# Optimization experiments

Hardware: AMD Instinct MI355X
Metric: run time of the kernel (lower is better)

Reference implementation:

```python
import jax, jax.numpy as jnp
import numpy as np

B, C, H, W = 4, 64, 64, 64

def setup_inputs() -> dict:
    key = jax.random.key(0)
    ks = jax.random.split(key, 8)
    s = 1.0 / np.sqrt(C)
    return {
        "x": jax.random.normal(ks[0], (B, C, H, W), dtype=jnp.float32),
        "Wq": jax.random.normal(ks[1], (C, C), dtype=jnp.float32) * s,
        "bq": jax.random.normal(ks[2], (C,), dtype=jnp.float32) * s,
        "Wk": jax.random.normal(ks[3], (C, C), dtype=jnp.float32) * s,
        "bk": jax.random.normal(ks[4], (C,), dtype=jnp.float32) * s,
        "Wv": jax.random.normal(ks[5], (C, C), dtype=jnp.float32) * s,
        "bv": jax.random.normal(ks[6], (C,), dtype=jnp.float32) * s,
        "gamma": jax.random.normal(ks[7], (1,), dtype=jnp.float32),
    }

def reference(x, Wq, bq, Wk, bk, Wv, bv, gamma):
    b, c, h, w = x.shape
    xf = x.reshape(b, c, h * w)                      # [B, C, N]
    q = jnp.einsum('oc,bcn->bon', Wq, xf) + bq[None, :, None]
    k = jnp.einsum('oc,bcn->bon', Wk, xf) + bk[None, :, None]
    v = jnp.einsum('oc,bcn->bon', Wv, xf) + bv[None, :, None]
    energy = jnp.einsum('bci,bcj->bij', q, k)        # [B, N, N] = Q^T K
    attn = jax.nn.softmax(energy, axis=-1)
    # out[b,c,i] = sum_j v[b,c,j] * attn[b,i,j]
    out = jnp.einsum('bcj,bij->bci', v, attn)        # [B, C, N]
    out = out.reshape(b, c, h, w)
    return gamma[0] * out + x
```

## Files before the change

kernel.cpp:

```cpp
#include <hip/hip_runtime.h>
#include <hip/hip_bf16.h>
#include <math.h>


constexpr int C_ = 64;
constexpr int N_ = 4096;
constexpr float LOG2E = 1.4426950408889634f;
constexpr float MBIAS = 86.5617f;

typedef float  f4 __attribute__((ext_vector_type(4)));
typedef short  s8 __attribute__((ext_vector_type(8)));

__device__ inline unsigned short f2bf(float x) {
    union { float f; unsigned u; } a; a.f = x;
    unsigned r = a.u + 0x7FFFu + ((a.u >> 16) & 1u);
    return (unsigned short)(r >> 16);
}
__device__ inline float bf2f(unsigned short h) {
    union { float f; unsigned u; } a; a.u = ((unsigned)h) << 16; return a.f;
}
__device__ inline uint4 pack8(const float* v) {
    uint4 r;
    r.x = (unsigned)f2bf(v[0]) | ((unsigned)f2bf(v[1]) << 16);
    r.y = (unsigned)f2bf(v[2]) | ((unsigned)f2bf(v[3]) << 16);
    r.z = (unsigned)f2bf(v[4]) | ((unsigned)f2bf(v[5]) << 16);
    r.w = (unsigned)f2bf(v[6]) | ((unsigned)f2bf(v[7]) << 16);
    return r;
}
__device__ inline void pack8_split(const float* v, uint4* hi, uint4* lo) {
    unsigned short h[8]; float rem[8];
    #pragma unroll
    for (int i = 0; i < 8; ++i) { h[i] = f2bf(v[i]); rem[i] = v[i] - bf2f(h[i]); }
    hi->x = (unsigned)h[0] | ((unsigned)h[1] << 16);
    hi->y = (unsigned)h[2] | ((unsigned)h[3] << 16);
    hi->z = (unsigned)h[4] | ((unsigned)h[5] << 16);
    hi->w = (unsigned)h[6] | ((unsigned)h[7] << 16);
    *lo = pack8(rem);
}
__device__ inline unsigned cvt_pk_bf16(float lo, float hi) {
    unsigned r;
    asm("v_cvt_pk_bf16_f32 %0, %1, %2" : "=v"(r) : "v"(lo), "v"(hi));
    return r;
}

__global__ __launch_bounds__(256) void prep_kernel(
    const float* __restrict__ x,
    const float* __restrict__ Wq, const float* __restrict__ bq,
    const float* __restrict__ Wk, const float* __restrict__ bk,
    const float* __restrict__ Wv, const float* __restrict__ bv,
    unsigned short* __restrict__ qhi, unsigned short* __restrict__ qlo,
    unsigned short* __restrict__ khi, unsigned short* __restrict__ klo,
    unsigned short* __restrict__ vv)
{
    __shared__ __align__(16) char smem[62208];
    float (*xs)[36]  = (float(*)[36])(smem);
    float (*wqs)[68] = (float(*)[68])(smem + 9216);
    float (*wks)[68] = (float(*)[68])(smem + 26624);
    float (*wvs)[68] = (float(*)[68])(smem + 44032);
    float* bias      = (float*)(smem + 61440);

    const int t    = threadIdx.x;
    const int nt2  = blockIdx.x, b = blockIdx.y;
    const int n0   = nt2 * 32;
    const int nt64 = nt2 >> 1, joff = (nt2 & 1) * 32;

    {
        const int nl = t & 31, cb = t >> 5;
        #pragma unroll
        for (int it = 0; it < 8; ++it) {
            int c = it * 8 + cb;
            xs[c][nl] = x[((long)b * 64 + c) * N_ + n0 + nl];
        }
        #pragma unroll
        for (int kk = 0; kk < 4; ++kk) {
            int f = t * 4 + kk * 1024;
            int o = f >> 6, c = f & 63;
            float4 w = *(const float4*)&Wq[f];
            wqs[c+0][o] = w.x; wqs[c+1][o] = w.y; wqs[c+2][o] = w.z; wqs[c+3][o] = w.w;
            w = *(const float4*)&Wk[f];
            wks[c+0][o] = w.x; wks[c+1][o] = w.y; wks[c+2][o] = w.z; wks[c+3][o] = w.w;
            w = *(const float4*)&Wv[f];
            wvs[c+0][o] = w.x; wvs[c+1][o] = w.y; wvs[c+2][o] = w.z; wvs[c+3][o] = w.w;
        }
        if (t < 64) { bias[t] = bq[t]; bias[64 + t] = bk[t]; bias[128 + t] = bv[t]; }
    }
    __syncthreads();

    const int o4 = (t & 15) * 4, n2 = (t >> 4) * 2;
    float aq[4][2], ak[4][2], av[4][2];
    #pragma unroll
    for (int oo = 0; oo < 4; ++oo) {
        aq[oo][0] = bias[o4 + oo];        aq[oo][1] = aq[oo][0];
        ak[oo][0] = bias[64 + o4 + oo];   ak[oo][1] = ak[oo][0];
        av[oo][0] = bias[128 + o4 + oo];  av[oo][1] = av[oo][0];
    }
    #pragma unroll 4
    for (int c = 0; c < 64; ++c) {
        float2 xv = *(const float2*)&xs[c][n2];
        f4 w1 = *(const f4*)&wqs[c][o4];
        f4 w2 = *(const f4*)&wks[c][o4];
        f4 w3 = *(const f4*)&wvs[c][o4];
        #pragma unroll
        for (int oo = 0; oo < 4; ++oo) {
            aq[oo][0] = fmaf(w1[oo], xv.x, aq[oo][0]);
            aq[oo][1] = fmaf(w1[oo], xv.y, aq[oo][1]);
            ak[oo][0] = fmaf(w2[oo], xv.x, ak[oo][0]);
            ak[oo][1] = fmaf(w2[oo], xv.y, ak[oo][1]);
            av[oo][0] = fmaf(w3[oo], xv.x, av[oo][0]);
            av[oo][1] = fmaf(w3[oo], xv.y, av[oo][1]);
        }
    }
    __syncthreads();

    {
        float (*qst)[68] = wqs;
        float (*kst)[68] = wks;
        float (*vst)[36] = xs;
        #pragma unroll
        for (int oo = 0; oo < 4; ++oo) {
            qst[n2][o4 + oo]     = aq[oo][0] * LOG2E;
            qst[n2 + 1][o4 + oo] = aq[oo][1] * LOG2E;
            kst[n2][o4 + oo]     = ak[oo][0];
            kst[n2 + 1][o4 + oo] = ak[oo][1];
            vst[o4 + oo][n2]     = av[oo][0];
            vst[o4 + oo][n2 + 1] = av[oo][1];
        }
    }
    __syncthreads();

    const long gbase = ((long)b * 64 + nt64) * 512;
    float tmp[8];
    {
        float (*qst)[68] = wqs;
        int mloc = t >> 7, ks = (t >> 6) & 1, L = t & 63;
        int m = (joff >> 4) + mloc;
        int rowl = mloc * 16 + (L & 15), c0 = ks * 32 + ((L >> 4) & 3) * 8;
        *(f4*)tmp       = *(const f4*)&qst[rowl][c0];
        *(f4*)(tmp + 4) = *(const f4*)&qst[rowl][c0 + 4];
        uint4 hi, lo; pack8_split(tmp, &hi, &lo);
        long ch = gbase + (m * 2 + ks) * 64 + L;
        *(uint4*)(qhi + ch * 8) = hi;
        *(uint4*)(qlo + ch * 8) = lo;
    }
    {
        float (*kst)[68] = wks;
        int cc = t >> 5, jl = t & 31;
        *(f4*)tmp       = *(const f4*)&kst[jl][cc * 8];
        *(f4*)(tmp + 4) = *(const f4*)&kst[jl][cc * 8 + 4];
        uint4 hi, lo; pack8_split(tmp, &hi, &lo);
        long ch = gbase + cc * 64 + joff + jl;
        *(uint4*)(khi + ch * 8) = hi;
        *(uint4*)(klo + ch * 8) = lo;
    }
    {
        float (*vst)[36] = xs;
        int cj = t >> 6, c = t & 63;
        *(f4*)tmp       = *(const f4*)&vst[c][cj * 8];
        *(f4*)(tmp + 4) = *(const f4*)&vst[c][cj * 8 + 4];
        long ch = gbase + ((joff >> 3) + cj) * 64 + c;
        *(uint4*)(vv + ch * 8) = pack8(tmp);
    }
}

__global__ __launch_bounds__(256, 4) void attn_kernel(
    const unsigned short* __restrict__ qhi, const unsigned short* __restrict__ qlo,
    const unsigned short* __restrict__ khi, const unsigned short* __restrict__ klo,
    const unsigned short* __restrict__ vv,
    unsigned* __restrict__ Opart, float* __restrict__ lpart,
    int njt, int Bn)
{
    __shared__ __align__(16) char pst_all[4 * 4608];

    const int t  = threadIdx.x;
    const int w  = t >> 6, L = t & 63;
    char* pst = pst_all + w * 4608;
    const int lh = L >> 4, ll = L & 15;
    const int ib2 = blockIdx.x * 4 + w;
    const int ib  = ib2 >> 1, mo = (ib2 & 1) * 2;
    const int jc = blockIdx.y, b = blockIdx.z;

    s8 qh[2][2], ql[2][2];
    {
        const int qb = (b * 64 + ib) * 512;
        #pragma unroll
        for (int m = 0; m < 2; ++m)
            #pragma unroll
            for (int ks = 0; ks < 2; ++ks) {
                int ch = qb + ((mo + m) * 2 + ks) * 64 + L;
                qh[m][ks] = *(const s8*)(qhi + (long)ch * 8);
                ql[m][ks] = *(const s8*)(qlo + (long)ch * 8);
            }
    }

    f4 O[2][4];
    #pragma unroll
    for (int m = 0; m < 2; ++m)
        #pragma unroll
        for (int nn = 0; nn < 4; ++nn) O[m][nn] = (f4){0.f, 0.f, 0.f, 0.f};
    float lps[2] = {0.f, 0.f};

    const int jt0 = jc * njt;
    for (int jt = 0; jt < njt; ++jt) {
        const int kb = (b * 64 + jt0 + jt) * 512;

        #pragma unroll
        for (int js = 0; js < 4; ++js) {
            __builtin_amdgcn_sched_barrier(0);
            s8 bh[2], bl[2];
            #pragma unroll
            for (int ks = 0; ks < 2; ++ks) {
                int ch = kb + (ks * 4 + lh) * 64 + js * 16 + ll;
                bh[ks] = *(const s8*)(khi + (long)ch * 8);
                bl[ks] = *(const s8*)(klo + (long)ch * 8);
            }
            #pragma unroll
            for (int m = 0; m < 2; ++m) {
                f4 acc = (f4){0.f, 0.f, 0.f, 0.f};
                acc = __builtin_amdgcn_mfma_f32_16x16x32_bf16(bh[0], qh[m][0], acc, 0, 0, 0);
                acc = __builtin_amdgcn_mfma_f32_16x16x32_bf16(bh[1], qh[m][1], acc, 0, 0, 0);
                acc = __builtin_amdgcn_mfma_f32_16x16x32_bf16(bl[0], qh[m][0], acc, 0, 0, 0);
                acc = __builtin_amdgcn_mfma_f32_16x16x32_bf16(bl[1], qh[m][1], acc, 0, 0, 0);
                acc = __builtin_amdgcn_mfma_f32_16x16x32_bf16(bh[0], ql[m][0], acc, 0, 0, 0);
                acc = __builtin_amdgcn_mfma_f32_16x16x32_bf16(bh[1], ql[m][1], acc, 0, 0, 0);
                float p0 = __builtin_amdgcn_exp2f(acc[0] - MBIAS);
                float p1 = __builtin_amdgcn_exp2f(acc[1] - MBIAS);
                float p2 = __builtin_amdgcn_exp2f(acc[2] - MBIAS);
                float p3 = __builtin_amdgcn_exp2f(acc[3] - MBIAS);
                lps[m] += (p0 + p1) + (p2 + p3);
                uint2 uu;
                uu.x = cvt_pk_bf16(p0, p1);
                uu.y = cvt_pk_bf16(p2, p3);
                *(uint2*)(pst + (m * 16 + ll) * 144 + (js * 16 + lh * 4) * 2) = uu;
            }
        }
        __builtin_amdgcn_sched_barrier(0);

        #pragma unroll
        for (int ks = 0; ks < 2; ++ks) {
            s8 bvf[4];
            #pragma unroll
            for (int nn = 0; nn < 4; ++nn) {
                int ch = kb + (ks * 4 + lh) * 64 + nn * 16 + ll;
                bvf[nn] = *(const s8*)(vv + (long)ch * 8);
            }
            #pragma unroll
            for (int m = 0; m < 2; ++m) {
                s8 ap = *(const s8*)(pst + (m * 16 + ll) * 144 + ks * 64 + lh * 16);
                #pragma unroll
                for (int nn = 0; nn < 4; ++nn)
                    O[m][nn] = __builtin_amdgcn_mfma_f32_16x16x32_bf16(ap, bvf[nn], O[m][nn], 0, 0, 0);
            }
        }
    }

    #pragma unroll
    for (int m = 0; m < 2; ++m) {
        float s = lps[m];
        s += __shfl_xor(s, 16);
        s += __shfl_xor(s, 32);
        lps[m] = s;
    }
    const long obase = ((long)jc * Bn + b) * 128 + ib2;
    if (lh == 0) {
        #pragma unroll
        for (int m = 0; m < 2; ++m)
            lpart[obase * 32 + m * 16 + ll] = lps[m];
    }
    unsigned* op = Opart + obase * 1024;
    #pragma unroll
    for (int m = 0; m < 2; ++m)
        #pragma unroll
        for (int nn = 0; nn < 4; ++nn)
            #pragma unroll
            for (int rh = 0; rh < 2; ++rh)
                op[((((m * 4 + nn) * 2) + rh) << 6) + L] =
                    cvt_pk_bf16(O[m][nn][rh * 2], O[m][nn][rh * 2 + 1]);
}

__global__ __launch_bounds__(512) void combine_kernel(
    const unsigned* __restrict__ Opart, const float* __restrict__ lpart,
    const float* __restrict__ x, const float* __restrict__ gamma_p,
    float* __restrict__ out, int js, int Bn)
{
    __shared__ float trn[64][36];
    __shared__ float lsc[32];
    const int t   = threadIdx.x;
    const int ib2 = blockIdx.x, b = blockIdx.y;
    const float g = gamma_p[0];

    float s[4] = {0.f, 0.f, 0.f, 0.f};
    for (int jc = 0; jc < js; ++jc) {
        const unsigned* base = Opart + (((long)jc * Bn + b) * 128 + ib2) * 1024;
        unsigned u0 = base[t];
        unsigned u1 = base[t + 512];
        s[0] += bf2f((unsigned short)(u0 & 0xffff));
        s[1] += bf2f((unsigned short)(u0 >> 16));
        s[2] += bf2f((unsigned short)(u1 & 0xffff));
        s[3] += bf2f((unsigned short)(u1 >> 16));
    }
    if (t < 32) {
        float ls = 0.f;
        for (int jc = 0; jc < js; ++jc)
            ls += lpart[(((long)jc * Bn + b) * 128 + ib2) * 32 + t];
        lsc[t] = g / ls;
    }
    #pragma unroll
    for (int e = 0; e < 2; ++e) {
        int u_idx = t + e * 512;
        int idx2 = u_idx >> 6, L = u_idx & 63;
        int m = idx2 >> 3, nn = (idx2 >> 1) & 3, rh = idx2 & 1;
        int col = nn * 16 + (L & 15);
        int row0 = m * 16 + (L >> 4) * 4 + rh * 2;
        trn[col][row0]     = s[e * 2 + 0];
        trn[col][row0 + 1] = s[e * 2 + 1];
    }
    __syncthreads();

    const int cl = t >> 3, nq = (t & 7) * 4;
    const long ob = ((long)b * 64 + cl) * N_ + ib2 * 32 + nq;
    float4 xr = *(const float4*)&x[ob];
    float4 rr;
    rr.x = trn[cl][nq + 0] * lsc[nq + 0] + xr.x;
    rr.y = trn[cl][nq + 1] * lsc[nq + 1] + xr.y;
    rr.z = trn[cl][nq + 2] * lsc[nq + 2] + xr.z;
    rr.w = trn[cl][nq + 3] * lsc[nq + 3] + xr.w;
    *(float4*)&out[ob] = rr;
}

extern "C" void kernel_launch(void* const* d_in, const int* in_sizes, int n_in,
                              void* d_out, int out_size, void* d_ws, size_t ws_size,
                              hipStream_t stream) {
    const float* x  = (const float*)d_in[0];
    const float* Wq = (const float*)d_in[1];
    const float* bq = (const float*)d_in[2];
    const float* Wk = (const float*)d_in[3];
    const float* bk = (const float*)d_in[4];
    const float* Wv = (const float*)d_in[5];
    const float* bv = (const float*)d_in[6];
    const float* gm = (const float*)d_in[7];
    float* out = (float*)d_out;

    const int B = in_sizes[0] / (C_ * N_);
    const size_t per = (size_t)B * N_ * C_;
    char* w = (char*)d_ws;
    unsigned short* qhi = (unsigned short*)w;
    unsigned short* qlo = qhi + per;
    unsigned short* khi = qlo + per;
    unsigned short* klo = khi + per;
    unsigned short* vv  = klo + per;
    size_t base = 5 * per * sizeof(unsigned short);

    int js = 8;
    while (js > 1) {
        size_t need = base + (size_t)js *
            ((size_t)B * 128 * 1024 * 4  + (size_t)B * 128 * 32 * 4 );
        if (need <= ws_size) break;
        js >>= 1;
    }
    unsigned* Opart = (unsigned*)(w + base);
    float* lpart = (float*)(w + base + (size_t)js * (size_t)B * 128 * 1024 * 4);

    prep_kernel<<<dim3(128, B), 256, 0, stream>>>(x, Wq, bq, Wk, bk, Wv, bv,
                                                  qhi, qlo, khi, klo, vv);
    attn_kernel<<<dim3(32, js, B), 256, 0, stream>>>(qhi, qlo, khi, klo, vv,
                                                     Opart, lpart, 64 / js, B);
    combine_kernel<<<dim3(128, B), 512, 0, stream>>>(Opart, lpart, x, gm, out, js, B);
}
```

Before: 133.0 us.

## Keep softmax probabilities in registers and feed PV via 16x16x16 MFMA

The probability tile no longer round-trips through LDS. The packed bf16 probabilities stay in registers in the QK accumulator layout and are used directly as the A operand of 16x16x16 bf16 MFMAs. V fragments are loaded in a matching 4-element layout. This removes LDS writes and reads and their latency, at the cost of twice as many half-width MFMA instructions, narrower V loads and more registers.

```diff
diff --git a/kernel.cpp b/kernel.cpp
--- a/kernel.cpp
+++ b/kernel.cpp
@@ -10,6 +10,7 @@
 
 typedef float  f4 __attribute__((ext_vector_type(4)));
 typedef short  s8 __attribute__((ext_vector_type(8)));
+typedef short  s4 __attribute__((ext_vector_type(4)));
 
 __device__ inline unsigned short f2bf(float x) {
     union { float f; unsigned u; } a; a.f = x;
@@ -42,6 +43,22 @@
     asm("v_cvt_pk_bf16_f32 %0, %1, %2" : "=v"(r) : "v"(lo), "v"(hi));
     return r;
 }
+
+#if __has_builtin(__builtin_amdgcn_mfma_f32_16x16x16_bf16)
+__device__ inline f4 mfma16(s4 a, s4 b, f4 c) {
+    return __builtin_amdgcn_mfma_f32_16x16x16_bf16(a, b, c, 0, 0, 0);
+}
+#elif __has_builtin(__builtin_amdgcn_mfma_f32_16x16x16bf16_1k)
+__device__ inline f4 mfma16(s4 a, s4 b, f4 c) {
+    return __builtin_amdgcn_mfma_f32_16x16x16bf16_1k(a, b, c, 0, 0, 0);
+}
+#else
+__device__ inline f4 mfma16(s4 a, s4 b, f4 c) {
+    s8 ap = {a[0], a[1], a[2], a[3], 0, 0, 0, 0};
+    s8 bp = {b[0], b[1], b[2], b[3], 0, 0, 0, 0};
+    return __builtin_amdgcn_mfma_f32_16x16x32_bf16(ap, bp, c, 0, 0, 0);
+}
+#endif
 
 __global__ __launch_bounds__(256) void prep_kernel(
     const float* __restrict__ x,
@@ -169,11 +186,8 @@
     unsigned* __restrict__ Opart, float* __restrict__ lpart,
     int njt, int Bn)
 {
-    __shared__ __align__(16) char pst_all[4 * 4608];
-
     const int t  = threadIdx.x;
     const int w  = t >> 6, L = t & 63;
-    char* pst = pst_all + w * 4608;
     const int lh = L >> 4, ll = L & 15;
     const int ib2 = blockIdx.x * 4 + w;
     const int ib  = ib2 >> 1, mo = (ib2 & 1) * 2;
@@ -202,6 +216,8 @@
     const int jt0 = jc * njt;
     for (int jt = 0; jt < njt; ++jt) {
         const int kb = (b * 64 + jt0 + jt) * 512;
+
+        uint2 pw[2][4];
 
         #pragma unroll
         for (int js = 0; js < 4; ++js) {
@@ -227,30 +243,29 @@
                 float p2 = __builtin_amdgcn_exp2f(acc[2] - MBIAS);
                 float p3 = __builtin_amdgcn_exp2f(acc[3] - MBIAS);
                 lps[m] += (p0 + p1) + (p2 + p3);
-                uint2 uu;
-                uu.x = cvt_pk_bf16(p0, p1);
-                uu.y = cvt_pk_bf16(p2, p3);
-                *(uint2*)(pst + (m * 16 + ll) * 144 + (js * 16 + lh * 4) * 2) = uu;
+                pw[m][js].x = cvt_pk_bf16(p0, p1);
+                pw[m][js].y = cvt_pk_bf16(p2, p3);
             }
         }
         __builtin_amdgcn_sched_barrier(0);
 
-        #pragma unroll
-        for (int ks = 0; ks < 2; ++ks) {
-            s8 bvf[4];
-            #pragma unroll
-            for (int nn = 0; nn < 4; ++nn) {
-                int ch = kb + (ks * 4 + lh) * 64 + nn * 16 + ll;
-                bvf[nn] = *(const s8*)(vv + (long)ch * 8);
-            }
-            #pragma unroll
-            for (int m = 0; m < 2; ++m) {
-                s8 ap = *(const s8*)(pst + (m * 16 + ll) * 144 + ks * 64 + lh * 16);
+        s4 vf[4][4];
+        {
+            const long vbase = ((long)kb + (lh >> 1) * 64 + ll) * 16 + (lh & 1) * 8;
+            #pragma unroll
+            for (int js2 = 0; js2 < 4; ++js2)
                 #pragma unroll
                 for (int nn = 0; nn < 4; ++nn)
-                    O[m][nn] = __builtin_amdgcn_mfma_f32_16x16x32_bf16(ap, bvf[nn], O[m][nn], 0, 0, 0);
-            }
-        }
+                    vf[js2][nn] = *(const s4*)((const char*)vv + vbase +
+                                               ((long)js2 * 128 + nn * 16) * 16);
+        }
+        #pragma unroll
+        for (int nn = 0; nn < 4; ++nn)
+            #pragma unroll
+            for (int m = 0; m < 2; ++m)
+                #pragma unroll
+                for (int js2 = 0; js2 < 4; ++js2)
+                    O[m][nn] = mfma16(*(const s4*)&pw[m][js2], vf[js2][nn], O[m][nn]);
     }
 
     #pragma unroll
```

New measurement: 128.3 us. 1.04x faster.
